# Kernel optimization log

Hardware: AMD Instinct MI355X
Metric: run time of the kernel (lower is better)

The kernel has to match this reference:

```python
import jax, jax.numpy as jnp
import numpy as np

N = 4096
D = 512   # d_model == dff (required by the original code path)
H = 4
NEG = -1e10
ALPHA = 0.3  # keras LeakyReLU default alpha


def setup_inputs() -> dict:
    key = jax.random.key(0)
    ks = jax.random.split(key, 8)
    nodes = jax.random.normal(ks[0], (N, D), dtype=jnp.float32)
    # sparse-ish 0/1 dense adjacency with self loops
    adj = (jax.random.uniform(ks[1], (N, N)) < 0.01).astype(jnp.float32)
    adj = jnp.maximum(adj, jnp.eye(N, dtype=jnp.float32))
    s = 0.05
    W_node = jax.random.normal(ks[2], (D, D), dtype=jnp.float32) * s
    b_node = jnp.zeros((D,), dtype=jnp.float32)
    K = jax.random.normal(ks[3], (H, D, D), dtype=jnp.float32) * s
    A_self = jax.random.normal(ks[4], (H, D), dtype=jnp.float32) * s
    A_neigh = jax.random.normal(ks[5], (H, D), dtype=jnp.float32) * s
    return {"nodes": nodes, "adj": adj, "W_node": W_node, "b_node": b_node,
            "K": K, "A_self": A_self, "A_neigh": A_neigh, "num_heads": H}


def reference(nodes, adj, W_node, b_node, K, A_self, A_neigh, num_heads):
    # node_layer: Dense(dff)
    x = nodes @ W_node + b_node                       # [N, D]
    # per-head projection, vectorized over heads
    feats = jnp.einsum('nd,hdf->hnf', x, K)           # [H, N, D]
    # additive attention scores; both terms are per-row scalars -> [H, N]
    s = jnp.einsum('hnf,hf->hn', feats, A_self) + jnp.einsum('hnf,hf->hn', feats, A_neigh)
    s = jnp.where(s > 0, s, ALPHA * s)                # LeakyReLU(alpha=0.3)
    # broadcast row score over columns + adjacency mask, softmax over neighbors
    logits = s[:, :, None] + NEG * (1.0 - adj)[None]  # [H, N, N]
    attn = jax.nn.softmax(logits, axis=-1)
    # dropout is identity at inference (training=False)
    out = jnp.einsum('hij,hjf->hif', attn, feats)     # [H, N, D]
    out = jnp.mean(out, axis=0)                       # mean over heads
    return jax.nn.relu(out)
```

## Files before the change

### kernel.cpp

```cpp
#include <hip/hip_runtime.h>


typedef short  short8 __attribute__((ext_vector_type(8)));
typedef float  f32x4  __attribute__((ext_vector_type(4)));

__device__ inline unsigned short f2bf(float f) {
    union { float f; unsigned int u; } v; v.f = f;
    unsigned int u = v.u;
    u += 0x7fffu + ((u >> 16) & 1u);
    return (unsigned short)(u >> 16);
}

__global__ __launch_bounds__(256) void kbarT_kernel(
        const float* __restrict__ K, unsigned short* __restrict__ KbarT,
        int D, int H, float invH) {
    __shared__ float tile[64][65];
    const int f0 = blockIdx.x * 64, d0 = blockIdx.y * 64;
    const int tid = threadIdx.x;
    const int c4 = (tid & 15) * 4;
    const int DD = D * D;

    for (int rr = tid >> 4; rr < 64; rr += 16) {
        float sx = 0.f, sy = 0.f, sz = 0.f, sw = 0.f;
        for (int h = 0; h < H; ++h) {
            float4 v = *reinterpret_cast<const float4*>(
                &K[(size_t)h * DD + (size_t)(d0 + rr) * D + f0 + c4]);
            sx += v.x; sy += v.y; sz += v.z; sw += v.w;
        }
        tile[rr][c4 + 0] = sx * invH;
        tile[rr][c4 + 1] = sy * invH;
        tile[rr][c4 + 2] = sz * invH;
        tile[rr][c4 + 3] = sw * invH;
    }
    __syncthreads();
    for (int fr = tid >> 4; fr < 64; fr += 16) {
        ushort4 o;
        o.x = f2bf(tile[c4 + 0][fr]);
        o.y = f2bf(tile[c4 + 1][fr]);
        o.z = f2bf(tile[c4 + 2][fr]);
        o.w = f2bf(tile[c4 + 3][fr]);
        *reinterpret_cast<ushort4*>(&KbarT[(size_t)(f0 + fr) * D + d0 + c4]) = o;
    }
}

template <bool CA, bool CB>
__device__ inline void gemm_body(const void* __restrict__ Ap,
                                 const void* __restrict__ Btp,
                                 const float* __restrict__ bias,
                                 unsigned short* __restrict__ C,
                                 int Nn, int K, int bx, int by) {
    __shared__ unsigned short As[64][32];
    __shared__ unsigned short Bs[64][32];
    const int tid  = threadIdx.x;
    const int lane = tid & 63;
    const int wave = tid >> 6;
    const int wy = wave >> 1, wx = wave & 1;
    const int row0 = by * 64, col0 = bx * 64;
    const int l15 = lane & 15, quad = lane >> 4;
    const int ldr = tid >> 2;
    const int ldk = (tid & 3) * 8;

    f32x4 acc[2][2] = {};

    for (int k0 = 0; k0 < K; k0 += 32) {
        short8 av, bv;
        if (CA) {
            const float* a = (const float*)Ap + (size_t)(row0 + ldr) * K + k0 + ldk;
            float4 x = *reinterpret_cast<const float4*>(a);
            float4 y = *reinterpret_cast<const float4*>(a + 4);
            av[0] = (short)f2bf(x.x); av[1] = (short)f2bf(x.y);
            av[2] = (short)f2bf(x.z); av[3] = (short)f2bf(x.w);
            av[4] = (short)f2bf(y.x); av[5] = (short)f2bf(y.y);
            av[6] = (short)f2bf(y.z); av[7] = (short)f2bf(y.w);
        } else {
            av = *reinterpret_cast<const short8*>(
                (const unsigned short*)Ap + (size_t)(row0 + ldr) * K + k0 + ldk);
        }
        if (CB) {
            const float* b = (const float*)Btp + (size_t)(col0 + ldr) * K + k0 + ldk;
            float4 x = *reinterpret_cast<const float4*>(b);
            float4 y = *reinterpret_cast<const float4*>(b + 4);
            bv[0] = (short)f2bf(x.x); bv[1] = (short)f2bf(x.y);
            bv[2] = (short)f2bf(x.z); bv[3] = (short)f2bf(x.w);
            bv[4] = (short)f2bf(y.x); bv[5] = (short)f2bf(y.y);
            bv[6] = (short)f2bf(y.z); bv[7] = (short)f2bf(y.w);
        } else {
            bv = *reinterpret_cast<const short8*>(
                (const unsigned short*)Btp + (size_t)(col0 + ldr) * K + k0 + ldk);
        }
        __syncthreads();
        *reinterpret_cast<short8*>(&As[ldr][ldk]) = av;
        *reinterpret_cast<short8*>(&Bs[ldr][ldk]) = bv;
        __syncthreads();
        short8 a0 = *reinterpret_cast<const short8*>(&As[wy * 32 +      l15][quad * 8]);
        short8 a1 = *reinterpret_cast<const short8*>(&As[wy * 32 + 16 + l15][quad * 8]);
        short8 b0 = *reinterpret_cast<const short8*>(&Bs[wx * 32 +      l15][quad * 8]);
        short8 b1 = *reinterpret_cast<const short8*>(&Bs[wx * 32 + 16 + l15][quad * 8]);
        acc[0][0] = __builtin_amdgcn_mfma_f32_16x16x32_bf16(a0, b0, acc[0][0], 0, 0, 0);
        acc[0][1] = __builtin_amdgcn_mfma_f32_16x16x32_bf16(a0, b1, acc[0][1], 0, 0, 0);
        acc[1][0] = __builtin_amdgcn_mfma_f32_16x16x32_bf16(a1, b0, acc[1][0], 0, 0, 0);
        acc[1][1] = __builtin_amdgcn_mfma_f32_16x16x32_bf16(a1, b1, acc[1][1], 0, 0, 0);
    }

#pragma unroll
    for (int mi = 0; mi < 2; ++mi)
#pragma unroll
        for (int ni = 0; ni < 2; ++ni) {
            int col = col0 + wx * 32 + ni * 16 + l15;
            float bvl = bias ? bias[col] : 0.f;
#pragma unroll
            for (int r = 0; r < 4; ++r) {
                int row = row0 + wy * 32 + mi * 16 + quad * 4 + r;
                C[(size_t)row * Nn + col] = f2bf(acc[mi][ni][r] + bvl);
            }
        }
}

__global__ __launch_bounds__(256) void gemm1_kernel(
        const unsigned short* __restrict__ KbarT, const float* __restrict__ W,
        const float* __restrict__ b, unsigned short* __restrict__ MmatT,
        float* __restrict__ bias2, int D, int gemmY) {
    if ((int)blockIdx.y >= gemmY) {
        int e = ((int)blockIdx.y - gemmY) * gridDim.x + blockIdx.x;
        int wave = threadIdx.x >> 6, lane = threadIdx.x & 63;
        int f = e * 4 + wave;
        if (f >= D) return;
        const unsigned short* kr = KbarT + (size_t)f * D + lane * 8;
        const float* br = b + lane * 8;
        float s = 0.f;
#pragma unroll
        for (int j = 0; j < 8; ++j) {
            union { unsigned int i; float f; } v; v.i = ((unsigned int)kr[j]) << 16;
            s += br[j] * v.f;
        }
#pragma unroll
        for (int off = 32; off; off >>= 1) s += __shfl_down(s, off, 64);
        if (lane == 0) bias2[f] = s;
        return;
    }
    gemm_body<false, true>(KbarT, W, nullptr, MmatT, D, D, blockIdx.x, blockIdx.y);
}

__global__ __launch_bounds__(256) void gemm2_kernel(
        const float* __restrict__ nodes, const unsigned short* __restrict__ MmatT,
        const float* __restrict__ bias2, unsigned short* __restrict__ g,
        int D, int K) {
    gemm_body<true, false>(nodes, MmatT, bias2, g, D, K, blockIdx.x, blockIdx.y);
}

__global__ __launch_bounds__(256) void aggregate_kernel(
        const float* __restrict__ adj, const unsigned short* __restrict__ g,
        float* __restrict__ out, int N, int D) {
    const int row = blockIdx.x;
    const int tid = threadIdx.x;
    __shared__ int lst[1024];
    __shared__ int cnt;
    if (tid == 0) cnt = 0;
    __syncthreads();

    const float* arow = adj + (size_t)row * N;
    const int nper = N >> 8;
    const int base = tid * nper;
    const float4* ap = reinterpret_cast<const float4*>(arow + base);
    for (int c = 0; c < (nper >> 2); ++c) {
        float4 a = ap[c];
        int b4 = base + c * 4;
        if (a.x > 0.5f) { int p = atomicAdd(&cnt, 1); if (p < 1024) lst[p] = b4;     }
        if (a.y > 0.5f) { int p = atomicAdd(&cnt, 1); if (p < 1024) lst[p] = b4 + 1; }
        if (a.z > 0.5f) { int p = atomicAdd(&cnt, 1); if (p < 1024) lst[p] = b4 + 2; }
        if (a.w > 0.5f) { int p = atomicAdd(&cnt, 1); if (p < 1024) lst[p] = b4 + 3; }
    }
    __syncthreads();
    int deg = cnt; if (deg > 1024) deg = 1024;

    const int col = tid * 2;
    float acc0 = 0.f, acc1 = 0.f;
    int k = 0;
    for (; k + 8 <= deg; k += 8) {
        unsigned int u[8];
#pragma unroll
        for (int j = 0; j < 8; ++j)
            u[j] = *reinterpret_cast<const unsigned int*>(&g[(size_t)lst[k + j] * D + col]);
#pragma unroll
        for (int j = 0; j < 8; ++j) {
            union { unsigned int i; float f; } lo, hi;
            lo.i = u[j] << 16; hi.i = u[j] & 0xffff0000u;
            acc0 += lo.f; acc1 += hi.f;
        }
    }
    for (; k < deg; ++k) {
        unsigned int u = *reinterpret_cast<const unsigned int*>(&g[(size_t)lst[k] * D + col]);
        union { unsigned int i; float f; } lo, hi;
        lo.i = u << 16; hi.i = u & 0xffff0000u;
        acc0 += lo.f; acc1 += hi.f;
    }

    float inv = deg > 0 ? 1.f / (float)deg : 0.f;
    acc0 *= inv; acc1 *= inv;
    float2 o;
    o.x = acc0 > 0.f ? acc0 : 0.f;
    o.y = acc1 > 0.f ? acc1 : 0.f;
    *reinterpret_cast<float2*>(&out[(size_t)row * D + col]) = o;
}

extern "C" void kernel_launch(void* const* d_in, const int* in_sizes, int n_in,
                              void* d_out, int out_size, void* d_ws, size_t ws_size,
                              hipStream_t stream) {
    const float* nodes  = (const float*)d_in[0];
    const float* adj    = (const float*)d_in[1];
    const float* W_node = (const float*)d_in[2];
    const float* b_node = (const float*)d_in[3];
    const float* K      = (const float*)d_in[4];

    const int D  = in_sizes[3];
    const int N  = in_sizes[0] / D;
    const int H  = in_sizes[4] / (D * D);
    const int DD = D * D;

    float* out = (float*)d_out;

    char* ws = (char*)d_ws;
    unsigned short* KbarT  = (unsigned short*)(ws);
    unsigned short* MmatT  = (unsigned short*)(ws + (size_t)DD * 2);
    unsigned short* g_bf16 = (unsigned short*)(ws + (size_t)DD * 4);
    float*          bias2  = (float*)        (ws + (size_t)DD * 4 + (size_t)N * D * 2);

    {
        dim3 grid(D / 64, D / 64);
        kbarT_kernel<<<grid, 256, 0, stream>>>(K, KbarT, D, H, 1.0f / (float)H);
    }

    {
        int gx = D / 64, gemmY = D / 64;
        int biasRows = (D / 4 + gx - 1) / gx;
        dim3 grid(gx, gemmY + biasRows);
        gemm1_kernel<<<grid, 256, 0, stream>>>(KbarT, W_node, b_node, MmatT, bias2, D, gemmY);
    }

    {
        dim3 grid(D / 64, N / 64);
        gemm2_kernel<<<grid, 256, 0, stream>>>(nodes, MmatT, bias2, g_bf16, D, D);
    }

    aggregate_kernel<<<N, 256, 0, stream>>>(adj, g_bf16, out, N, D);
}
```

Baseline: 163.7 us.

## Fuse all stages into one cooperative persistent kernel with grid syncs

Replaces the four separate launches (Kbar transpose, weight GEMM plus bias, node GEMM, aggregation) with one cooperative kernel of 1024 blocks separated by grid-wide barriers. The head-mean is folded directly into the first GEMM's A-tile load, nodes are pre-cast to bf16 in parallel, and the node GEMM stages tiles through LDS with direct global-to-LDS loads. The goal is to remove launch gaps and the KbarT intermediate. The cost is two grid syncs, idle blocks in the phases that use fewer blocks, and a dependence on all 1024 blocks being co-resident.

```diff
diff --git a/kernel.cpp b/kernel.cpp
--- a/kernel.cpp
+++ b/kernel.cpp
@@ -1,4 +1,7 @@
 #include <hip/hip_runtime.h>
+#include <hip/hip_cooperative_groups.h>
+
+namespace cg = cooperative_groups;
 
 
 typedef short  short8 __attribute__((ext_vector_type(8)));
@@ -11,196 +14,205 @@
     return (unsigned short)(u >> 16);
 }
 
-__global__ __launch_bounds__(256) void kbarT_kernel(
-        const float* __restrict__ K, unsigned short* __restrict__ KbarT,
-        int D, int H, float invH) {
-    __shared__ float tile[64][65];
-    const int f0 = blockIdx.x * 64, d0 = blockIdx.y * 64;
-    const int tid = threadIdx.x;
-    const int c4 = (tid & 15) * 4;
-    const int DD = D * D;
-
-    for (int rr = tid >> 4; rr < 64; rr += 16) {
-        float sx = 0.f, sy = 0.f, sz = 0.f, sw = 0.f;
-        for (int h = 0; h < H; ++h) {
-            float4 v = *reinterpret_cast<const float4*>(
-                &K[(size_t)h * DD + (size_t)(d0 + rr) * D + f0 + c4]);
-            sx += v.x; sy += v.y; sz += v.z; sw += v.w;
-        }
-        tile[rr][c4 + 0] = sx * invH;
-        tile[rr][c4 + 1] = sy * invH;
-        tile[rr][c4 + 2] = sz * invH;
-        tile[rr][c4 + 3] = sw * invH;
-    }
-    __syncthreads();
-    for (int fr = tid >> 4; fr < 64; fr += 16) {
-        ushort4 o;
-        o.x = f2bf(tile[c4 + 0][fr]);
-        o.y = f2bf(tile[c4 + 1][fr]);
-        o.z = f2bf(tile[c4 + 2][fr]);
-        o.w = f2bf(tile[c4 + 3][fr]);
-        *reinterpret_cast<ushort4*>(&KbarT[(size_t)(f0 + fr) * D + d0 + c4]) = o;
-    }
-}
-
-template <bool CA, bool CB>
-__device__ inline void gemm_body(const void* __restrict__ Ap,
-                                 const void* __restrict__ Btp,
-                                 const float* __restrict__ bias,
-                                 unsigned short* __restrict__ C,
-                                 int Nn, int K, int bx, int by) {
+__device__ inline void gl_lds16(const void* gp, void* lp) {
+    __builtin_amdgcn_global_load_lds(
+        (const __attribute__((address_space(1))) void*)gp,
+        (__attribute__((address_space(3))) void*)lp, 16, 0, 0);
+}
+
+__global__ __launch_bounds__(256, 4) void fused_gat(
+        const float* __restrict__ nodes, const float* __restrict__ adj,
+        const float* __restrict__ W, const float* __restrict__ b,
+        const float* __restrict__ K,
+        unsigned short* __restrict__ MmatT, float* __restrict__ bias2,
+        unsigned short* __restrict__ nodesBf, unsigned short* __restrict__ g,
+        float* __restrict__ out, int N, int D, int H) {
     __shared__ unsigned short As[64][32];
     __shared__ unsigned short Bs[64][32];
-    const int tid  = threadIdx.x;
-    const int lane = tid & 63;
-    const int wave = tid >> 6;
-    const int wy = wave >> 1, wx = wave & 1;
-    const int row0 = by * 64, col0 = bx * 64;
-    const int l15 = lane & 15, quad = lane >> 4;
-    const int ldr = tid >> 2;
-    const int ldk = (tid & 3) * 8;
-
-    f32x4 acc[2][2] = {};
-
-    for (int k0 = 0; k0 < K; k0 += 32) {
-        short8 av, bv;
-        if (CA) {
-            const float* a = (const float*)Ap + (size_t)(row0 + ldr) * K + k0 + ldk;
-            float4 x = *reinterpret_cast<const float4*>(a);
-            float4 y = *reinterpret_cast<const float4*>(a + 4);
-            av[0] = (short)f2bf(x.x); av[1] = (short)f2bf(x.y);
-            av[2] = (short)f2bf(x.z); av[3] = (short)f2bf(x.w);
-            av[4] = (short)f2bf(y.x); av[5] = (short)f2bf(y.y);
-            av[6] = (short)f2bf(y.z); av[7] = (short)f2bf(y.w);
-        } else {
-            av = *reinterpret_cast<const short8*>(
-                (const unsigned short*)Ap + (size_t)(row0 + ldr) * K + k0 + ldk);
-        }
-        if (CB) {
-            const float* b = (const float*)Btp + (size_t)(col0 + ldr) * K + k0 + ldk;
-            float4 x = *reinterpret_cast<const float4*>(b);
-            float4 y = *reinterpret_cast<const float4*>(b + 4);
-            bv[0] = (short)f2bf(x.x); bv[1] = (short)f2bf(x.y);
-            bv[2] = (short)f2bf(x.z); bv[3] = (short)f2bf(x.w);
-            bv[4] = (short)f2bf(y.x); bv[5] = (short)f2bf(y.y);
-            bv[6] = (short)f2bf(y.z); bv[7] = (short)f2bf(y.w);
-        } else {
-            bv = *reinterpret_cast<const short8*>(
-                (const unsigned short*)Btp + (size_t)(col0 + ldr) * K + k0 + ldk);
-        }
-        __syncthreads();
-        *reinterpret_cast<short8*>(&As[ldr][ldk]) = av;
-        *reinterpret_cast<short8*>(&Bs[ldr][ldk]) = bv;
-        __syncthreads();
-        short8 a0 = *reinterpret_cast<const short8*>(&As[wy * 32 +      l15][quad * 8]);
-        short8 a1 = *reinterpret_cast<const short8*>(&As[wy * 32 + 16 + l15][quad * 8]);
-        short8 b0 = *reinterpret_cast<const short8*>(&Bs[wx * 32 +      l15][quad * 8]);
-        short8 b1 = *reinterpret_cast<const short8*>(&Bs[wx * 32 + 16 + l15][quad * 8]);
-        acc[0][0] = __builtin_amdgcn_mfma_f32_16x16x32_bf16(a0, b0, acc[0][0], 0, 0, 0);
-        acc[0][1] = __builtin_amdgcn_mfma_f32_16x16x32_bf16(a0, b1, acc[0][1], 0, 0, 0);
-        acc[1][0] = __builtin_amdgcn_mfma_f32_16x16x32_bf16(a1, b0, acc[1][0], 0, 0, 0);
-        acc[1][1] = __builtin_amdgcn_mfma_f32_16x16x32_bf16(a1, b1, acc[1][1], 0, 0, 0);
-    }
-
-#pragma unroll
-    for (int mi = 0; mi < 2; ++mi)
-#pragma unroll
-        for (int ni = 0; ni < 2; ++ni) {
-            int col = col0 + wx * 32 + ni * 16 + l15;
-            float bvl = bias ? bias[col] : 0.f;
-#pragma unroll
-            for (int r = 0; r < 4; ++r) {
-                int row = row0 + wy * 32 + mi * 16 + quad * 4 + r;
-                C[(size_t)row * Nn + col] = f2bf(acc[mi][ni][r] + bvl);
-            }
-        }
-}
-
-__global__ __launch_bounds__(256) void gemm1_kernel(
-        const unsigned short* __restrict__ KbarT, const float* __restrict__ W,
-        const float* __restrict__ b, unsigned short* __restrict__ MmatT,
-        float* __restrict__ bias2, int D, int gemmY) {
-    if ((int)blockIdx.y >= gemmY) {
-        int e = ((int)blockIdx.y - gemmY) * gridDim.x + blockIdx.x;
-        int wave = threadIdx.x >> 6, lane = threadIdx.x & 63;
-        int f = e * 4 + wave;
-        if (f >= D) return;
-        const unsigned short* kr = KbarT + (size_t)f * D + lane * 8;
-        const float* br = b + lane * 8;
-        float s = 0.f;
-#pragma unroll
-        for (int j = 0; j < 8; ++j) {
-            union { unsigned int i; float f; } v; v.i = ((unsigned int)kr[j]) << 16;
-            s += br[j] * v.f;
-        }
-#pragma unroll
-        for (int off = 32; off; off >>= 1) s += __shfl_down(s, off, 64);
-        if (lane == 0) bias2[f] = s;
-        return;
-    }
-    gemm_body<false, true>(KbarT, W, nullptr, MmatT, D, D, blockIdx.x, blockIdx.y);
-}
-
-__global__ __launch_bounds__(256) void gemm2_kernel(
-        const float* __restrict__ nodes, const unsigned short* __restrict__ MmatT,
-        const float* __restrict__ bias2, unsigned short* __restrict__ g,
-        int D, int K) {
-    gemm_body<true, false>(nodes, MmatT, bias2, g, D, K, blockIdx.x, blockIdx.y);
-}
-
-__global__ __launch_bounds__(256) void aggregate_kernel(
-        const float* __restrict__ adj, const unsigned short* __restrict__ g,
-        float* __restrict__ out, int N, int D) {
-    const int row = blockIdx.x;
-    const int tid = threadIdx.x;
+    __shared__ float red[4][64];
     __shared__ int lst[1024];
     __shared__ int cnt;
-    if (tid == 0) cnt = 0;
-    __syncthreads();
-
-    const float* arow = adj + (size_t)row * N;
-    const int nper = N >> 8;
-    const int base = tid * nper;
-    const float4* ap = reinterpret_cast<const float4*>(arow + base);
-    for (int c = 0; c < (nper >> 2); ++c) {
-        float4 a = ap[c];
-        int b4 = base + c * 4;
-        if (a.x > 0.5f) { int p = atomicAdd(&cnt, 1); if (p < 1024) lst[p] = b4;     }
-        if (a.y > 0.5f) { int p = atomicAdd(&cnt, 1); if (p < 1024) lst[p] = b4 + 1; }
-        if (a.z > 0.5f) { int p = atomicAdd(&cnt, 1); if (p < 1024) lst[p] = b4 + 2; }
-        if (a.w > 0.5f) { int p = atomicAdd(&cnt, 1); if (p < 1024) lst[p] = b4 + 3; }
+
+    const int bid  = blockIdx.x;
+    const int tid  = threadIdx.x;
+    const int NB   = gridDim.x;
+    const int DD   = D * D;
+    const int lane = tid & 63, wave = tid >> 6;
+    const int wy = wave >> 1, wx = wave & 1;
+    const int l15 = lane & 15, quad = lane >> 4;
+
+    if (bid < 64) {
+        const int by = bid >> 3, bx = bid & 7;
+        const int f0 = by * 64, d0 = bx * 64;
+        const float invH = 1.0f / (float)H;
+        const int kk = tid >> 3;
+        const int ff = (tid & 7) * 8;
+        const int dr = tid >> 2;
+        const int dk = (tid & 3) * 8;
+        f32x4 acc[2][2] = {};
+        for (int k0 = 0; k0 < D; k0 += 32) {
+            float s[8] = {0.f, 0.f, 0.f, 0.f, 0.f, 0.f, 0.f, 0.f};
+            for (int h = 0; h < H; ++h) {
+                const float* kp = K + ((size_t)h * D + (k0 + kk)) * D + f0 + ff;
+                float4 x = *reinterpret_cast<const float4*>(kp);
+                float4 y = *reinterpret_cast<const float4*>(kp + 4);
+                s[0] += x.x; s[1] += x.y; s[2] += x.z; s[3] += x.w;
+                s[4] += y.x; s[5] += y.y; s[6] += y.z; s[7] += y.w;
+            }
+            const float* wp = W + (size_t)(d0 + dr) * D + k0 + dk;
+            float4 u = *reinterpret_cast<const float4*>(wp);
+            float4 v = *reinterpret_cast<const float4*>(wp + 4);
+            short8 bv;
+            bv[0] = (short)f2bf(u.x); bv[1] = (short)f2bf(u.y);
+            bv[2] = (short)f2bf(u.z); bv[3] = (short)f2bf(u.w);
+            bv[4] = (short)f2bf(v.x); bv[5] = (short)f2bf(v.y);
+            bv[6] = (short)f2bf(v.z); bv[7] = (short)f2bf(v.w);
+            __syncthreads();
+#pragma unroll
+            for (int j = 0; j < 8; ++j)
+                As[ff + j][kk] = f2bf(s[j] * invH);
+            *reinterpret_cast<short8*>(&Bs[dr][dk]) = bv;
+            __syncthreads();
+            short8 a0 = *reinterpret_cast<const short8*>(&As[wy * 32 +      l15][quad * 8]);
+            short8 a1 = *reinterpret_cast<const short8*>(&As[wy * 32 + 16 + l15][quad * 8]);
+            short8 b0 = *reinterpret_cast<const short8*>(&Bs[wx * 32 +      l15][quad * 8]);
+            short8 b1 = *reinterpret_cast<const short8*>(&Bs[wx * 32 + 16 + l15][quad * 8]);
+            acc[0][0] = __builtin_amdgcn_mfma_f32_16x16x32_bf16(a0, b0, acc[0][0], 0, 0, 0);
+            acc[0][1] = __builtin_amdgcn_mfma_f32_16x16x32_bf16(a0, b1, acc[0][1], 0, 0, 0);
+            acc[1][0] = __builtin_amdgcn_mfma_f32_16x16x32_bf16(a1, b0, acc[1][0], 0, 0, 0);
+            acc[1][1] = __builtin_amdgcn_mfma_f32_16x16x32_bf16(a1, b1, acc[1][1], 0, 0, 0);
+        }
+#pragma unroll
+        for (int mi = 0; mi < 2; ++mi)
+#pragma unroll
+            for (int ni = 0; ni < 2; ++ni) {
+                int col = d0 + wx * 32 + ni * 16 + l15;
+#pragma unroll
+                for (int r = 0; r < 4; ++r) {
+                    int row = f0 + wy * 32 + mi * 16 + quad * 4 + r;
+                    MmatT[(size_t)row * D + col] = f2bf(acc[mi][ni][r]);
+                }
+            }
+    } else if (bid < 72) {
+        const int f0 = (bid - 64) * 64;
+        const int fl = tid & 63, grp = tid >> 6;
+        const float invH = 1.0f / (float)H;
+        float a = 0.f;
+        for (int d = grp; d < D; d += 4) {
+            const float* kp = K + (size_t)d * D + f0 + fl;
+            float v = 0.f;
+#pragma unroll
+            for (int h = 0; h < 4; ++h) v += kp[(size_t)h * DD];
+            a += b[d] * v;
+        }
+        red[grp][fl] = a;
+        __syncthreads();
+        if (tid < 64)
+            bias2[f0 + tid] = (red[0][tid] + red[1][tid] + red[2][tid] + red[3][tid]) * invH;
+    } else {
+        const int total  = (N * D) >> 3;
+        const int stride = (NB - 72) << 8;
+        for (int i = (bid - 72) * 256 + tid; i < total; i += stride) {
+            const float* p = nodes + (size_t)i * 8;
+            float4 x = *reinterpret_cast<const float4*>(p);
+            float4 y = *reinterpret_cast<const float4*>(p + 4);
+            short8 o;
+            o[0] = (short)f2bf(x.x); o[1] = (short)f2bf(x.y);
+            o[2] = (short)f2bf(x.z); o[3] = (short)f2bf(x.w);
+            o[4] = (short)f2bf(y.x); o[5] = (short)f2bf(y.y);
+            o[6] = (short)f2bf(y.z); o[7] = (short)f2bf(y.w);
+            *reinterpret_cast<short8*>(nodesBf + (size_t)i * 8) = o;
+        }
     }
-    __syncthreads();
-    int deg = cnt; if (deg > 1024) deg = 1024;
-
-    const int col = tid * 2;
-    float acc0 = 0.f, acc1 = 0.f;
-    int k = 0;
-    for (; k + 8 <= deg; k += 8) {
-        unsigned int u[8];
-#pragma unroll
-        for (int j = 0; j < 8; ++j)
-            u[j] = *reinterpret_cast<const unsigned int*>(&g[(size_t)lst[k + j] * D + col]);
-#pragma unroll
-        for (int j = 0; j < 8; ++j) {
+    cg::this_grid().sync();
+
+    if (bid < 512) {
+        const int by = bid >> 3, bx = bid & 7;
+        const unsigned short* Ag = nodesBf + (size_t)(by * 64 + (tid >> 2)) * D + (tid & 3) * 8;
+        const unsigned short* Bg = MmatT   + (size_t)(bx * 64 + (tid >> 2)) * D + (tid & 3) * 8;
+        unsigned short* AsW = &As[0][0] + wave * 512;
+        unsigned short* BsW = &Bs[0][0] + wave * 512;
+        f32x4 acc[2][2] = {};
+        for (int k0 = 0; k0 < D; k0 += 32) {
+            __syncthreads();
+            gl_lds16(Ag + k0, AsW);
+            gl_lds16(Bg + k0, BsW);
+            asm volatile("s_waitcnt vmcnt(0)" ::: "memory");
+            __syncthreads();
+            short8 a0 = *reinterpret_cast<const short8*>(&As[wy * 32 +      l15][quad * 8]);
+            short8 a1 = *reinterpret_cast<const short8*>(&As[wy * 32 + 16 + l15][quad * 8]);
+            short8 b0 = *reinterpret_cast<const short8*>(&Bs[wx * 32 +      l15][quad * 8]);
+            short8 b1 = *reinterpret_cast<const short8*>(&Bs[wx * 32 + 16 + l15][quad * 8]);
+            acc[0][0] = __builtin_amdgcn_mfma_f32_16x16x32_bf16(a0, b0, acc[0][0], 0, 0, 0);
+            acc[0][1] = __builtin_amdgcn_mfma_f32_16x16x32_bf16(a0, b1, acc[0][1], 0, 0, 0);
+            acc[1][0] = __builtin_amdgcn_mfma_f32_16x16x32_bf16(a1, b0, acc[1][0], 0, 0, 0);
+            acc[1][1] = __builtin_amdgcn_mfma_f32_16x16x32_bf16(a1, b1, acc[1][1], 0, 0, 0);
+        }
+#pragma unroll
+        for (int mi = 0; mi < 2; ++mi)
+#pragma unroll
+            for (int ni = 0; ni < 2; ++ni) {
+                int col = bx * 64 + wx * 32 + ni * 16 + l15;
+                float bvl = bias2[col];
+#pragma unroll
+                for (int r = 0; r < 4; ++r) {
+                    int row = by * 64 + wy * 32 + mi * 16 + quad * 4 + r;
+                    g[(size_t)row * D + col] = f2bf(acc[mi][ni][r] + bvl);
+                }
+            }
+    }
+    cg::this_grid().sync();
+
+    const int rows_per = N / NB;
+    for (int rr = 0; rr < rows_per; ++rr) {
+        const int row = bid * rows_per + rr;
+        if (tid == 0) cnt = 0;
+        __syncthreads();
+        const float* arow = adj + (size_t)row * N;
+        const int nper = N >> 8;
+        const int base = tid * nper;
+        const float4* ap = reinterpret_cast<const float4*>(arow + base);
+        for (int c = 0; c < (nper >> 2); ++c) {
+            float4 a = ap[c];
+            int b4 = base + c * 4;
+            if (a.x > 0.5f) { int p = atomicAdd(&cnt, 1); if (p < 1024) lst[p] = b4;     }
+            if (a.y > 0.5f) { int p = atomicAdd(&cnt, 1); if (p < 1024) lst[p] = b4 + 1; }
+            if (a.z > 0.5f) { int p = atomicAdd(&cnt, 1); if (p < 1024) lst[p] = b4 + 2; }
+            if (a.w > 0.5f) { int p = atomicAdd(&cnt, 1); if (p < 1024) lst[p] = b4 + 3; }
+        }
+        __syncthreads();
+        int deg = cnt; if (deg > 1024) deg = 1024;
+
+        const int col = tid * 2;
+        float acc0 = 0.f, acc1 = 0.f;
+        int k2 = 0;
+        for (; k2 + 8 <= deg; k2 += 8) {
+            unsigned int u[8];
+#pragma unroll
+            for (int j = 0; j < 8; ++j)
+                u[j] = *reinterpret_cast<const unsigned int*>(&g[(size_t)lst[k2 + j] * D + col]);
+#pragma unroll
+            for (int j = 0; j < 8; ++j) {
+                union { unsigned int i; float f; } lo, hi;
+                lo.i = u[j] << 16; hi.i = u[j] & 0xffff0000u;
+                acc0 += lo.f; acc1 += hi.f;
+            }
+        }
+        for (; k2 < deg; ++k2) {
+            unsigned int u = *reinterpret_cast<const unsigned int*>(&g[(size_t)lst[k2] * D + col]);
             union { unsigned int i; float f; } lo, hi;
-            lo.i = u[j] << 16; hi.i = u[j] & 0xffff0000u;
+            lo.i = u << 16; hi.i = u & 0xffff0000u;
             acc0 += lo.f; acc1 += hi.f;
         }
+
+        float inv = deg > 0 ? 1.f / (float)deg : 0.f;
+        acc0 *= inv; acc1 *= inv;
+        float2 o;
+        o.x = acc0 > 0.f ? acc0 : 0.f;
+        o.y = acc1 > 0.f ? acc1 : 0.f;
+        *reinterpret_cast<float2*>(&out[(size_t)row * D + col]) = o;
+        __syncthreads();
     }
-    for (; k < deg; ++k) {
-        unsigned int u = *reinterpret_cast<const unsigned int*>(&g[(size_t)lst[k] * D + col]);
-        union { unsigned int i; float f; } lo, hi;
-        lo.i = u << 16; hi.i = u & 0xffff0000u;
-        acc0 += lo.f; acc1 += hi.f;
-    }
-
-    float inv = deg > 0 ? 1.f / (float)deg : 0.f;
-    acc0 *= inv; acc1 *= inv;
-    float2 o;
-    o.x = acc0 > 0.f ? acc0 : 0.f;
-    o.y = acc1 > 0.f ? acc1 : 0.f;
-    *reinterpret_cast<float2*>(&out[(size_t)row * D + col]) = o;
 }
 
 extern "C" void kernel_launch(void* const* d_in, const int* in_sizes, int n_in,
@@ -220,27 +232,15 @@
     float* out = (float*)d_out;
 
     char* ws = (char*)d_ws;
-    unsigned short* KbarT  = (unsigned short*)(ws);
-    unsigned short* MmatT  = (unsigned short*)(ws + (size_t)DD * 2);
-    unsigned short* g_bf16 = (unsigned short*)(ws + (size_t)DD * 4);
-    float*          bias2  = (float*)        (ws + (size_t)DD * 4 + (size_t)N * D * 2);
-
-    {
-        dim3 grid(D / 64, D / 64);
-        kbarT_kernel<<<grid, 256, 0, stream>>>(K, KbarT, D, H, 1.0f / (float)H);
-    }
-
-    {
-        int gx = D / 64, gemmY = D / 64;
-        int biasRows = (D / 4 + gx - 1) / gx;
-        dim3 grid(gx, gemmY + biasRows);
-        gemm1_kernel<<<grid, 256, 0, stream>>>(KbarT, W_node, b_node, MmatT, bias2, D, gemmY);
-    }
-
-    {
-        dim3 grid(D / 64, N / 64);
-        gemm2_kernel<<<grid, 256, 0, stream>>>(nodes, MmatT, bias2, g_bf16, D, D);
-    }
-
-    aggregate_kernel<<<N, 256, 0, stream>>>(adj, g_bf16, out, N, D);
-}
+    unsigned short* MmatT   = (unsigned short*)(ws);
+    float*          bias2   = (float*)        (ws + (size_t)DD * 2);
+    unsigned short* nodesBf = (unsigned short*)(ws + (size_t)DD * 2 + (size_t)D * 4);
+    unsigned short* g_bf16  = (unsigned short*)(ws + (size_t)DD * 2 + (size_t)D * 4
+                                                   + (size_t)N * D * 2);
+
+    void* args[] = { (void*)&nodes, (void*)&adj, (void*)&W_node, (void*)&b_node,
+                     (void*)&K, (void*)&MmatT, (void*)&bias2, (void*)&nodesBf,
+                     (void*)&g_bf16, (void*)&out,
+                     (void*)&N, (void*)&D, (void*)&H };
+    hipLaunchCooperativeKernel(fused_gat, dim3(1024), dim3(256), args, 0, stream);
+}
```

Result: slower. 425.8 us (+160.2%).
